# Kernel tuning notes

Hardware: AMD Instinct MI355X
Metric: run time of the kernel (lower is better)

## Reference

```python
import math
import jax, jax.numpy as jnp
import numpy as np

LMAX = 6
SH_DIM = (LMAX + 1) ** 2
NUM_INV = LMAX + 1
SILU_SCALE = 1.0 / 0.6  # ScaledSiLU


def scaled_silu(x):
    return jax.nn.silu(x) * SILU_SCALE


def sph_harm(v):
    """Real spherical harmonics up to LMAX, 'component' normalization, input normalized. [*, 3] -> [*, SH_DIM]."""
    n = jnp.sqrt(jnp.sum(v * v, axis=-1, keepdims=True) + 1e-12)
    v = v / n
    x, y, z = v[..., 0], v[..., 1], v[..., 2]
    st = jnp.sqrt(jnp.clip(x * x + y * y, 0.0, None))  # sin(theta)
    phi = jnp.arctan2(y, x)
    # fully-normalized associated Legendre P[(l,m)] via standard recurrences
    P = {(0, 0): jnp.full_like(z, math.sqrt(1.0 / (4.0 * math.pi)))}
    for m in range(1, LMAX + 1):
        P[(m, m)] = -math.sqrt((2 * m + 1) / (2.0 * m)) * st * P[(m - 1, m - 1)]
    for m in range(0, LMAX):
        P[(m + 1, m)] = math.sqrt(2 * m + 3) * z * P[(m, m)]
    for m in range(0, LMAX + 1):
        for l in range(m + 2, LMAX + 1):
            a = math.sqrt((4 * l * l - 1.0) / (l * l - m * m))
            b = math.sqrt(((l - 1) ** 2 - m * m) / (4.0 * (l - 1) ** 2 - 1.0))
            P[(l, m)] = a * (z * P[(l - 1, m)] - b * P[(l - 2, m)])
    s4pi = math.sqrt(4.0 * math.pi)
    sq2 = math.sqrt(2.0)
    cols = []
    for l in range(LMAX + 1):
        for m in range(-l, l + 1):
            if m < 0:
                cols.append(s4pi * sq2 * P[(l, -m)] * jnp.sin(-m * phi))
            elif m == 0:
                cols.append(s4pi * P[(l, 0)])
            else:
                cols.append(s4pi * sq2 * P[(l, m)] * jnp.cos(m * phi))
    return jnp.stack(cols, axis=-1)


def sh_bilinear_inv(sh1, sh2):
    """Per-l mean of elementwise product. [E, SH_DIM] x2 -> [E, NUM_INV]."""
    outs, idx = [], 0
    for l in range(LMAX + 1):
        d = 2 * l + 1
        outs.append(jnp.mean(sh1[:, idx:idx + d] * sh2[:, idx:idx + d], axis=-1))
        idx += d
    return jnp.stack(outs, axis=-1)


def _forward(node_scalar, node_vector, edge_rbf, edge_udiff, edge_index,
             W_edge, b_edge, W_x1, b_x1, W_x2, b_x2, ln_g, ln_b, W_inv, b_inv):
    H = node_scalar.shape[1]
    N = node_scalar.shape[0]
    j, i = edge_index[0], edge_index[1]
    inv_sqrt3 = 1.0 / math.sqrt(3.0)
    inv_sqrt_h = 1.0 / math.sqrt(H)

    rbf_h = edge_rbf @ W_edge + b_edge  # [E, 3H]

    # scatter-mean of edge directions onto receiving nodes
    counts = jax.ops.segment_sum(jnp.ones_like(i, dtype=edge_udiff.dtype), i, num_segments=N)
    ref_vec = jax.ops.segment_sum(edge_udiff, i, num_segments=N) / jnp.maximum(counts, 1.0)[:, None]
    ref_norm = jnp.sqrt(jnp.sum(ref_vec * ref_vec, axis=-1, keepdims=True) + 1e-9)
    ref_vec = ref_vec / ref_norm
    zero_mask = ref_norm[:, 0] < 5e-5
    default_vec = jnp.array([1.0, 0.0, 0.0], dtype=ref_vec.dtype)
    ref_vec = jnp.where(zero_mask[:, None], default_vec, ref_vec)

    edge_sh = sph_harm(edge_udiff)          # [E, SH_DIM]
    ref_sh = sph_harm(ref_vec)[i]           # [E, SH_DIM]
    inv = sh_bilinear_inv(edge_sh, ref_sh)  # [E, NUM_INV]
    mu = jnp.mean(inv, axis=-1, keepdims=True)
    var = jnp.var(inv, axis=-1, keepdims=True)
    inv = (inv - mu) / jnp.sqrt(var + 1e-5) * ln_g + ln_b

    cos_theta = jnp.sum(edge_udiff * ref_vec[i], axis=-1, keepdims=True)  # [E,1]
    geom = jnp.concatenate([cos_theta, inv], axis=-1)  # [E, NUM_INV+1]
    gate = jnp.tanh(scaled_silu(geom @ W_inv + b_inv))
    rbf_h = rbf_h * (1.0 + gate)

    scalar_proj = scaled_silu(node_scalar @ W_x1 + b_x1) @ W_x2 + b_x2  # [N, 3H]
    x_ji = scalar_proj[j] * rbf_h * inv_sqrt3
    x1, x2, x3 = x_ji[:, :H], x_ji[:, H:2 * H], x_ji[:, 2 * H:]

    vec_ji = (x1[:, None, :] * node_vector[j] + x2[:, None, :] * edge_udiff[:, :, None]) * inv_sqrt_h  # [E,3,H]
    delta_vector = jax.ops.segment_sum(vec_ji, i, num_segments=N)
    delta_scalar = jax.ops.segment_sum(x3, i, num_segments=N)
    return delta_scalar, delta_vector


def setup_inputs() -> dict:
    N, E, H, R = 50000, 400000, 64, 64
    key = jax.random.key(0)
    ks = jax.random.split(key, 16)
    ud = jax.random.normal(ks[3], (E, 3), dtype=jnp.float32)
    ud = ud / jnp.linalg.norm(ud, axis=-1, keepdims=True)
    s = 0.05
    return {
        "node_scalar": jax.random.normal(ks[0], (N, H), dtype=jnp.float32),
        "node_vector": jax.random.normal(ks[1], (N, 3, H), dtype=jnp.float32),
        "edge_rbf": jax.random.uniform(ks[2], (E, R), dtype=jnp.float32),
        "edge_udiff": ud,
        "edge_index": jax.random.randint(ks[4], (2, E), 0, N, dtype=jnp.int32),
        "W_edge": jax.random.normal(ks[5], (R, 3 * H), dtype=jnp.float32) * s,
        "b_edge": jnp.zeros((3 * H,), dtype=jnp.float32),
        "W_x1": jax.random.normal(ks[6], (H, H // 2), dtype=jnp.float32) * s,
        "b_x1": jnp.zeros((H // 2,), dtype=jnp.float32),
        "W_x2": jax.random.normal(ks[7], (H // 2, 3 * H), dtype=jnp.float32) * s,
        "b_x2": jnp.zeros((3 * H,), dtype=jnp.float32),
        "ln_g": jnp.ones((NUM_INV,), dtype=jnp.float32),
        "ln_b": jnp.zeros((NUM_INV,), dtype=jnp.float32),
        "W_inv": jax.random.normal(ks[8], (NUM_INV + 1, 3 * H), dtype=jnp.float32) * s,
        "b_inv": jnp.zeros((3 * H,), dtype=jnp.float32),
    }


def reference(node_scalar, node_vector, edge_rbf, edge_udiff, edge_index,
              W_edge, b_edge, W_x1, b_x1, W_x2, b_x2, ln_g, ln_b, W_inv, b_inv):
    return _forward(node_scalar, node_vector, edge_rbf, edge_udiff, edge_index,
                    W_edge, b_edge, W_x1, b_x1, W_x2, b_x2, ln_g, ln_b, W_inv, b_inv)
```

## Files before the change

kernel.cpp:

```cpp
#include <hip/hip_runtime.h>
#include <math.h>

#define LMAXX 6
#define TPB 256
#define TILE_E 64
#define SCB 256
#define CAPS 12

typedef __attribute__((ext_vector_type(8))) short short8v;
typedef __attribute__((ext_vector_type(16))) float f32x16;
union FragU { short8v v; uint2 u2[2]; };

__device__ __forceinline__ unsigned pack_bf16(float a, float b) {
    unsigned ua = __float_as_uint(a);
    unsigned ub = __float_as_uint(b);
    ua += 0x7fffu + ((ua >> 16) & 1u);
    ub += 0x7fffu + ((ub >> 16) & 1u);
    return (ua >> 16) | (ub & 0xffff0000u);
}
__device__ __forceinline__ float bf16_lo(unsigned w) { return __uint_as_float(w << 16); }
__device__ __forceinline__ float bf16_hi(unsigned w) { return __uint_as_float(w & 0xffff0000u); }

__device__ __forceinline__ void dirang(float x, float y, float z,
                                       float& zo, float& st, float& cphi, float& sphi) {
    float nn = sqrtf(x * x + y * y + z * z + 1e-12f);
    float iv = 1.0f / nn;
    x *= iv; y *= iv; zo = z * iv;
    float st2 = x * x + y * y;
    st = sqrtf(st2 > 0.f ? st2 : 0.f);
    if (st > 1e-30f) { cphi = x / st; sphi = y / st; }
    else { cphi = 1.0f; sphi = 0.0f; }
}

__device__ __forceinline__ void legP(float z, float st, float P[7][7]) {
    P[0][0] = 0.28209479177387814f;
#pragma unroll
    for (int m = 1; m <= LMAXX; ++m)
        P[m][m] = -sqrtf((2.f * m + 1.f) / (2.f * m)) * st * P[m - 1][m - 1];
#pragma unroll
    for (int m = 0; m < LMAXX; ++m)
        P[m + 1][m] = sqrtf(2.f * m + 3.f) * z * P[m][m];
#pragma unroll
    for (int m = 0; m <= LMAXX; ++m) {
#pragma unroll
        for (int l = m + 2; l <= LMAXX; ++l) {
            float a = sqrtf((4.f * l * l - 1.f) / (float)(l * l - m * m));
            float b = sqrtf((float)((l - 1) * (l - 1) - m * m) /
                            (4.f * (l - 1) * (l - 1) - 1.f));
            P[l][m] = a * (z * P[l - 1][m] - b * P[l - 2][m]);
        }
    }
}

__global__ void k_hist(const int* __restrict__ eidx, int* __restrict__ icnt, int E) {
    int e = blockIdx.x * blockDim.x + threadIdx.x;
    if (e >= E) return;
    atomicAdd(&icnt[eidx[E + e]], 1);
}

__global__ void k_scan1(const int* __restrict__ icnt, int* __restrict__ offs,
                        int* __restrict__ bsum, int N) {
    __shared__ int s[SCB];
    int t = threadIdx.x;
    int idx = blockIdx.x * SCB + t;
    int v = (idx < N) ? icnt[idx] : 0;
    s[t] = v; __syncthreads();
#pragma unroll
    for (int off = 1; off < SCB; off <<= 1) {
        int u = (t >= off) ? s[t - off] : 0;
        __syncthreads();
        s[t] += u;
        __syncthreads();
    }
    if (idx < N) offs[idx] = s[t] - v;
    if (t == SCB - 1) bsum[blockIdx.x] = s[t];
}

__global__ void k_scan2(int* __restrict__ bsum, int nb) {
    __shared__ int s[1024];
    int t = threadIdx.x;
    int v = (t < nb) ? bsum[t] : 0;
    s[t] = v; __syncthreads();
#pragma unroll
    for (int off = 1; off < 1024; off <<= 1) {
        int u = (t >= off) ? s[t - off] : 0;
        __syncthreads();
        s[t] += u;
        __syncthreads();
    }
    if (t < nb) bsum[t] = s[t] - v;
}

__global__ void k_scan3(int* __restrict__ offs, const int* __restrict__ bsum,
                        int* __restrict__ cursor, int N) {
    int idx = blockIdx.x * SCB + threadIdx.x;
    if (idx >= N) return;
    int o = offs[idx] + bsum[blockIdx.x];
    offs[idx] = o;
    cursor[idx] = o;
}

__global__ void k_perm(const float* __restrict__ ud, const int* __restrict__ eidx,
                       int* __restrict__ cursor, int* __restrict__ perm,
                       int* __restrict__ ii_s, int* __restrict__ jj_s,
                       float* __restrict__ ud_s, int E) {
    int e = blockIdx.x * blockDim.x + threadIdx.x;
    if (e >= E) return;
    int i = eidx[E + e];
    int j = eidx[e];
    int pos = atomicAdd(&cursor[i], 1);
    perm[pos] = e;
    ii_s[pos] = i;
    jj_s[pos] = j;
    ud_s[3 * pos + 0] = ud[3 * e + 0];
    ud_s[3 * pos + 1] = ud[3 * e + 1];
    ud_s[3 * pos + 2] = ud[3 * e + 2];
}

__global__ void k_node_ref(const int* __restrict__ offs, const int* __restrict__ icnt,
                           const float* __restrict__ ud_s,
                           float* __restrict__ ref_vec, int N) {
    int n = blockIdx.x * blockDim.x + threadIdx.x;
    if (n >= N) return;
    int o0 = offs[n], c = icnt[n];
    float sx = 0.f, sy = 0.f, sz = 0.f;
    for (int e = o0; e < o0 + c; ++e) {
        sx += ud_s[3 * e + 0];
        sy += ud_s[3 * e + 1];
        sz += ud_s[3 * e + 2];
    }
    float d = fmaxf((float)c, 1.0f);
    float vx = sx / d, vy = sy / d, vz = sz / d;
    float norm = sqrtf(vx * vx + vy * vy + vz * vz + 1e-9f);
    float ivn = 1.0f / norm;
    vx *= ivn; vy *= ivn; vz *= ivn;
    if (norm < 5e-5f) { vx = 1.f; vy = 0.f; vz = 0.f; }
    ref_vec[3 * n + 0] = vx;
    ref_vec[3 * n + 1] = vy;
    ref_vec[3 * n + 2] = vz;
}

__global__ __launch_bounds__(TPB) void k_sprojv(const float* __restrict__ ns,
                                                const float* __restrict__ W1,
                                                const float* __restrict__ b1,
                                                const float* __restrict__ W2,
                                                const float* __restrict__ b2,
                                                const float* __restrict__ nvec,
                                                unsigned* __restrict__ gat, int N) {
    __shared__ float sW1[64 * 32];
    __shared__ float sW2[32 * 192];
    __shared__ float sb2[192];
    __shared__ float sb1[32];
    __shared__ float sbuf[4][64];
    __shared__ float h1buf[4][32];
    int t = threadIdx.x;
    for (int p = t; p < 64 * 32; p += TPB) sW1[p] = W1[p];
    for (int p = t; p < 32 * 192; p += TPB) sW2[p] = W2[p];
    if (t < 192) sb2[t] = b2[t];
    if (t < 32) sb1[t] = b1[t];

    int w = t >> 6, l = t & 63;
    int nwaves = gridDim.x * 4;
    int iters = (N + nwaves - 1) / nwaves;
    for (int it = 0; it < iters; ++it) {
        int n = blockIdx.x * 4 + w + it * nwaves;
        bool act = n < N;
        __syncthreads();
        if (act) sbuf[w][l] = ns[(size_t)n * 64 + l];
        __syncthreads();
        if (act) {
            int k = l & 31;
            float h = sb1[k];
#pragma unroll
            for (int c = 0; c < 64; ++c) h = fmaf(sbuf[w][c], sW1[c * 32 + k], h);
            float sig = 1.0f / (1.0f + __expf(-h));
            h = h * sig * (1.0f / 0.6f);
            if (l < 32) h1buf[w][l] = h;
        }
        __syncthreads();
        if (act) {
            float a[3];
#pragma unroll
            for (int m = 0; m < 3; ++m) {
                int o = l + 64 * m;
                float acc = sb2[o];
#pragma unroll
                for (int kk = 0; kk < 32; ++kk)
                    acc = fmaf(h1buf[w][kk], sW2[kk * 192 + o], acc);
                a[m] = acc;
            }
            size_t nb = (size_t)n * 192;
            float nv0 = nvec[nb + l];
            float nv1 = nvec[nb + 64 + l];
            float nv2 = nvec[nb + 128 + l];
            gat[nb + l]        = pack_bf16(a[0], a[1]);
            gat[nb + 64 + l]   = pack_bf16(a[2], nv0);
            gat[nb + 128 + l]  = pack_bf16(nv1, nv2);
        }
    }
}

__global__ void k_geom_s(const float* __restrict__ ud_s, const int* __restrict__ ii_s,
                         const float* __restrict__ ref_vec,
                         const float* __restrict__ ln_g, const float* __restrict__ ln_b,
                         float* __restrict__ geom_s, int E) {
    int r = blockIdx.x * blockDim.x + threadIdx.x;
    if (r >= E) return;
    int i = ii_s[r];
    float ux = ud_s[3 * r], uy = ud_s[3 * r + 1], uz = ud_s[3 * r + 2];
    float rvx = ref_vec[3 * i], rvy = ref_vec[3 * i + 1], rvz = ref_vec[3 * i + 2];

    float zE, stE, cpE, spE, zR, stR, cpR, spR;
    dirang(ux, uy, uz, zE, stE, cpE, spE);
    dirang(rvx, rvy, rvz, zR, stR, cpR, spR);

    float Pe[7][7], Pr[7][7];
    legP(zE, stE, Pe);
    legP(zR, stR, Pr);

    float cmE[7], smE[7], cmR[7], smR[7];
    cmE[0] = 1.f; smE[0] = 0.f; cmE[1] = cpE; smE[1] = spE;
    cmR[0] = 1.f; smR[0] = 0.f; cmR[1] = cpR; smR[1] = spR;
#pragma unroll
    for (int m = 2; m <= LMAXX; ++m) {
        cmE[m] = 2.f * cpE * cmE[m - 1] - cmE[m - 2];
        smE[m] = 2.f * cpE * smE[m - 1] - smE[m - 2];
        cmR[m] = 2.f * cpR * cmR[m - 1] - cmR[m - 2];
        smR[m] = 2.f * cpR * smR[m - 1] - smR[m - 2];
    }

    float inv[7];
#pragma unroll
    for (int l = 0; l <= LMAXX; ++l) inv[l] = Pe[l][0] * Pr[l][0];
#pragma unroll
    for (int m = 1; m <= LMAXX; ++m) {
        float cross = cmE[m] * cmR[m] + smE[m] * smR[m];
#pragma unroll
        for (int l = m; l <= LMAXX; ++l)
            inv[l] += 2.f * Pe[l][m] * Pr[l][m] * cross;
    }
    const float fourpi = 12.566370614359172f;
#pragma unroll
    for (int l = 0; l <= LMAXX; ++l) inv[l] *= fourpi / (float)(2 * l + 1);

    float mu = 0.f;
#pragma unroll
    for (int l = 0; l < 7; ++l) mu += inv[l];
    mu *= (1.0f / 7.0f);
    float var = 0.f;
#pragma unroll
    for (int l = 0; l < 7; ++l) { float d = inv[l] - mu; var += d * d; }
    var *= (1.0f / 7.0f);
    float rstd = rsqrtf(var + 1e-5f);
    float ct = ux * rvx + uy * rvy + uz * rvz;
    float* g = geom_s + (size_t)r * 8;
    g[0] = ct;
#pragma unroll
    for (int l = 0; l < 7; ++l) g[1 + l] = (inv[l] - mu) * rstd * ln_g[l] + ln_b[l];
}

__global__ __launch_bounds__(TPB, 4) void k_main(
    const float* __restrict__ rbf, const float* __restrict__ W_edge,
    const float* __restrict__ b_edge, const float* __restrict__ W_inv,
    const float* __restrict__ b_inv, const float* __restrict__ geom_s,
    const unsigned* __restrict__ gat, const float* __restrict__ ud_s,
    const int* __restrict__ ii_s, const int* __restrict__ jj_s,
    const int* __restrict__ perm,
    float* __restrict__ dscal, float* __restrict__ dvec, int E) {
    __shared__ __align__(16) unsigned sWT[192 * 34];
    __shared__ int sii[64];
    __shared__ int sslot[64];
    __shared__ int sfirst[64];
    __shared__ int sD;
    __shared__ float sacc[CAPS * 256];

    int t = threadIdx.x;
    int l = t & 63;
    int wid = t >> 6;
    int eh = wid >> 1;
    int wc = wid & 1;
    int lo5 = l & 31;
    int hi = l >> 5;
    int h = wc * 32 + lo5;

    for (int p = t; p < 192 * 32; p += TPB) {
        int col = p >> 5, kd = p & 31;
        sWT[col * 34 + kd] = pack_bf16(W_edge[(2 * kd) * 192 + col],
                                       W_edge[(2 * kd + 1) * 192 + col]);
    }

    float wv_inv[8][3];
#pragma unroll
    for (int c = 0; c < 8; ++c)
#pragma unroll
        for (int q = 0; q < 3; ++q)
            wv_inv[c][q] = W_inv[c * 192 + q * 64 + h];
    float bi[3], be[3];
#pragma unroll
    for (int q = 0; q < 3; ++q) {
        bi[q] = b_inv[q * 64 + h];
        be[q] = b_edge[q * 64 + h];
    }

    const float inv_sqrt3 = 0.57735026918962584f;
    const float inv_sqrt_h = 0.125f;

    int ntiles = (E + TILE_E - 1) / TILE_E;
    for (int tile = blockIdx.x; tile < ntiles; tile += gridDim.x) {
        int e0 = tile * TILE_E;
        __syncthreads();
        if (t < 64) {
            int rg = e0 + t;
            sii[t] = (rg < E) ? ii_s[rg] : -1;
        }
        __syncthreads();

        if (t < 64) {
            bool flag = (t == 0) || (sii[t] != sii[t - 1]);
            unsigned long long bal = __ballot(flag);
            unsigned long long mask =
                (t == 63) ? ~0ull : ((1ull << (t + 1)) - 1ull);
            int slot = __popcll(bal & mask) - 1;
            sslot[t] = slot;
            if (flag) sfirst[slot] = t;
            if (t == 0) sD = __popcll(bal);
        }

        FragU afr[4];
        int arow = lo5 + 32 * eh;
        int rga = e0 + arow;
        if (rga < E) {
            int row = perm[rga];
            const float4* rp = (const float4*)&rbf[(size_t)row * 64 + hi * 8];
#pragma unroll
            for (int ks = 0; ks < 4; ++ks) {
                float4 f0 = rp[ks * 4];
                float4 f1 = rp[ks * 4 + 1];
                afr[ks].u2[0] = make_uint2(pack_bf16(f0.x, f0.y), pack_bf16(f0.z, f0.w));
                afr[ks].u2[1] = make_uint2(pack_bf16(f1.x, f1.y), pack_bf16(f1.z, f1.w));
            }
        } else {
#pragma unroll
            for (int ks = 0; ks < 4; ++ks) {
                afr[ks].u2[0] = make_uint2(0u, 0u);
                afr[ks].u2[1] = make_uint2(0u, 0u);
            }
        }

        f32x16 acc0 = {0.f,0.f,0.f,0.f,0.f,0.f,0.f,0.f,0.f,0.f,0.f,0.f,0.f,0.f,0.f,0.f};
        f32x16 acc1 = acc0, acc2 = acc0;
        int bc0 = (wc * 32 + lo5) * 34;
#pragma unroll
        for (int ks = 0; ks < 4; ++ks) {
            int off = ks * 8 + hi * 4;
            FragU b0, b1, b2;
            b0.u2[0] = *(const uint2*)&sWT[bc0 + off];
            b0.u2[1] = *(const uint2*)&sWT[bc0 + off + 2];
            b1.u2[0] = *(const uint2*)&sWT[bc0 + 64 * 34 + off];
            b1.u2[1] = *(const uint2*)&sWT[bc0 + 64 * 34 + off + 2];
            b2.u2[0] = *(const uint2*)&sWT[bc0 + 128 * 34 + off];
            b2.u2[1] = *(const uint2*)&sWT[bc0 + 128 * 34 + off + 2];
            acc0 = __builtin_amdgcn_mfma_f32_32x32x16_bf16(afr[ks].v, b0.v, acc0, 0, 0, 0);
            acc1 = __builtin_amdgcn_mfma_f32_32x32x16_bf16(afr[ks].v, b1.v, acc1, 0, 0, 0);
            acc2 = __builtin_amdgcn_mfma_f32_32x32x16_bf16(afr[ks].v, b2.v, acc2, 0, 0, 0);
        }

        __syncthreads();
        int D = sD;
        bool slotmode = (D <= CAPS);
        if (slotmode) {
            for (int p = t; p < D * 256; p += TPB) sacc[p] = 0.f;
        }
        __syncthreads();

        float a_s = 0.f, a_v0 = 0.f, a_v1 = 0.f, a_v2 = 0.f;
        int runi = -1, runslot = -1;
        auto flush = [&]() {
            if (runi < 0) return;
            if (slotmode) {
                float* sa = &sacc[runslot * 256];
                atomicAdd(&sa[h], a_s);
                atomicAdd(&sa[64 + h], a_v0);
                atomicAdd(&sa[128 + h], a_v1);
                atomicAdd(&sa[192 + h], a_v2);
            } else {
                atomicAdd(&dscal[(size_t)runi * 64 + h], a_s);
                atomicAdd(&dvec[(size_t)runi * 192 + h], a_v0);
                atomicAdd(&dvec[(size_t)runi * 192 + 64 + h], a_v1);
                atomicAdd(&dvec[(size_t)runi * 192 + 128 + h], a_v2);
            }
        };
#pragma unroll
        for (int r = 0; r < 16; ++r) {
            int el = eh * 32 + (r & 3) + 8 * (r >> 2) + 4 * hi;
            int rg = e0 + el;
            if (rg < E) {
                int i = sii[el];
                int j = jj_s[rg];
                if (i != runi) {
                    flush();
                    a_s = 0.f; a_v0 = 0.f; a_v1 = 0.f; a_v2 = 0.f;
                    runi = i; runslot = sslot[el];
                }
                const float4* gp = (const float4*)(geom_s + (size_t)rg * 8);
                float4 g0 = gp[0];
                float4 g1 = gp[1];
                float u0 = bi[0], u1 = bi[1], u2 = bi[2];
                float gg[8] = {g0.x, g0.y, g0.z, g0.w, g1.x, g1.y, g1.z, g1.w};
#pragma unroll
                for (int c = 0; c < 8; ++c) {
                    u0 = fmaf(gg[c], wv_inv[c][0], u0);
                    u1 = fmaf(gg[c], wv_inv[c][1], u1);
                    u2 = fmaf(gg[c], wv_inv[c][2], u2);
                }
                float gate[3];
                float uu[3] = {u0, u1, u2};
#pragma unroll
                for (int q = 0; q < 3; ++q) {
                    float u = uu[q];
                    float sig = 1.0f / (1.0f + __expf(-u));
                    float v = u * sig * (1.0f / 0.6f);
                    v = fminf(fmaxf(v, -20.f), 20.f);
                    float e2v = __expf(2.0f * v);
                    gate[q] = (e2v - 1.0f) / (e2v + 1.0f);
                }
                size_t jb = (size_t)j * 192;
                unsigned w0 = gat[jb + h];
                unsigned w1 = gat[jb + 64 + h];
                unsigned w2 = gat[jb + 128 + h];
                float sp0 = bf16_lo(w0), sp1 = bf16_hi(w0), sp2 = bf16_lo(w1);
                float nv0 = bf16_hi(w1), nv1 = bf16_lo(w2), nv2 = bf16_hi(w2);
                float x1 = sp0 * (acc0[r] + be[0]) * (1.0f + gate[0]) * inv_sqrt3;
                float x2 = sp1 * (acc1[r] + be[1]) * (1.0f + gate[1]) * inv_sqrt3;
                float x3 = sp2 * (acc2[r] + be[2]) * (1.0f + gate[2]) * inv_sqrt3;
                a_s += x3;
                float ud0 = ud_s[3 * rg + 0];
                float ud1 = ud_s[3 * rg + 1];
                float ud2 = ud_s[3 * rg + 2];
                a_v0 += (x1 * nv0 + x2 * ud0) * inv_sqrt_h;
                a_v1 += (x1 * nv1 + x2 * ud1) * inv_sqrt_h;
                a_v2 += (x1 * nv2 + x2 * ud2) * inv_sqrt_h;
            }
        }
        flush();
        __syncthreads();

        if (slotmode) {
            int Dreal = D - ((sii[63] < 0) ? 1 : 0);
            for (int s = 0; s < D; ++s) {
                int n = sii[sfirst[s]];
                if (n < 0) continue;
                float val = sacc[s * 256 + t];
                bool boundary = (s == 0) || (s == Dreal - 1);
                float* ptr = (t < 64) ? &dscal[(size_t)n * 64 + t]
                                      : &dvec[(size_t)n * 192 + (t - 64)];
                if (boundary) atomicAdd(ptr, val);
                else *ptr = val;
            }
        }
    }
}

extern "C" void kernel_launch(void* const* d_in, const int* in_sizes, int n_in,
                              void* d_out, int out_size, void* d_ws, size_t ws_size,
                              hipStream_t stream) {
    const float* node_scalar = (const float*)d_in[0];
    const float* node_vector = (const float*)d_in[1];
    const float* edge_rbf    = (const float*)d_in[2];
    const float* edge_udiff  = (const float*)d_in[3];
    const int*   edge_index  = (const int*)d_in[4];
    const float* W_edge      = (const float*)d_in[5];
    const float* b_edge      = (const float*)d_in[6];
    const float* W_x1        = (const float*)d_in[7];
    const float* b_x1        = (const float*)d_in[8];
    const float* W_x2        = (const float*)d_in[9];
    const float* b_x2        = (const float*)d_in[10];
    const float* ln_g        = (const float*)d_in[11];
    const float* ln_b        = (const float*)d_in[12];
    const float* W_inv       = (const float*)d_in[13];
    const float* b_inv       = (const float*)d_in[14];

    int N = in_sizes[0] / 64;
    int E = in_sizes[3] / 3;

    float* ws = (float*)d_ws;
    size_t o = 0;
    auto A4 = [&]() { o = (o + 3) & ~(size_t)3; };
    int*      icnt   = (int*)(ws + o); o += N; A4();
    int*      offs   = (int*)(ws + o); o += N; A4();
    int*      cursor = (int*)(ws + o); o += N; A4();
    int*      bsum   = (int*)(ws + o); o += 1024; A4();
    float*    ref_vec= ws + o; o += (size_t)N * 3; A4();
    unsigned* gat    = (unsigned*)(ws + o); o += (size_t)N * 192; A4();
    int*      perm   = (int*)(ws + o); o += E; A4();
    float*    geom_s = ws + o; o += (size_t)E * 8; A4();
    float*    ud_s   = ws + o; o += (size_t)E * 3; A4();
    int*      ii_s   = (int*)(ws + o); o += E; A4();
    int*      jj_s   = (int*)(ws + o); o += E; A4();

    float* dscal = (float*)d_out;
    float* dvec  = (float*)d_out + (size_t)N * 64;

    hipMemsetAsync(icnt, 0, (size_t)N * sizeof(int), stream);
    hipMemsetAsync(d_out, 0, (size_t)out_size * sizeof(float), stream);

    int nb = (N + SCB - 1) / SCB;

    k_hist<<<(E + TPB - 1) / TPB, TPB, 0, stream>>>(edge_index, icnt, E);
    k_scan1<<<nb, SCB, 0, stream>>>(icnt, offs, bsum, N);
    k_scan2<<<1, 1024, 0, stream>>>(bsum, nb);
    k_scan3<<<nb, SCB, 0, stream>>>(offs, bsum, cursor, N);
    k_perm<<<(E + TPB - 1) / TPB, TPB, 0, stream>>>(edge_udiff, edge_index, cursor,
                                                    perm, ii_s, jj_s, ud_s, E);
    k_node_ref<<<(N + TPB - 1) / TPB, TPB, 0, stream>>>(offs, icnt, ud_s, ref_vec, N);
    k_sprojv<<<512, TPB, 0, stream>>>(node_scalar, W_x1, b_x1, W_x2, b_x2,
                                      node_vector, gat, N);
    k_geom_s<<<(E + TPB - 1) / TPB, TPB, 0, stream>>>(ud_s, ii_s, ref_vec,
                                                      ln_g, ln_b, geom_s, E);
    k_main<<<1024, TPB, 0, stream>>>(edge_rbf, W_edge, b_edge, W_inv, b_inv, geom_s,
                                     gat, ud_s, ii_s, jj_s, perm, dscal, dvec, E);
}
```

Measured before the change: 576.2 us.

## Compute invariant gate via MFMA and pack per-edge sorted data into structs

Moves the per-edge W_inv projection of the geometric invariants onto bf16 MFMA instructions, computes the gate factors once per tile, and stores them packed as bf16. Geometric features are stored as bf16 instead of fp32. The separate sorted arrays (perm, ii, jj, udiff) are merged into one 32-byte struct per edge so each edge needs fewer scattered loads. A small kernel pre-packs W_inv to bf16. The aim is less redundant per-lane FMA and transcendental work and less memory traffic, at the cost of bf16 precision on the gate and geometry values.

```diff
diff --git a/kernel.cpp b/kernel.cpp
--- a/kernel.cpp
+++ b/kernel.cpp
@@ -9,7 +9,7 @@
 
 typedef __attribute__((ext_vector_type(8))) short short8v;
 typedef __attribute__((ext_vector_type(16))) float f32x16;
-union FragU { short8v v; uint2 u2[2]; };
+union FragU { short8v v; uint2 u2[2]; uint4 u4; };
 
 __device__ __forceinline__ unsigned pack_bf16(float a, float b) {
     unsigned ua = __float_as_uint(a);
@@ -101,33 +101,30 @@
 }
 
 __global__ void k_perm(const float* __restrict__ ud, const int* __restrict__ eidx,
-                       int* __restrict__ cursor, int* __restrict__ perm,
-                       int* __restrict__ ii_s, int* __restrict__ jj_s,
-                       float* __restrict__ ud_s, int E) {
+                       int* __restrict__ cursor, uint4* __restrict__ estr, int E) {
     int e = blockIdx.x * blockDim.x + threadIdx.x;
     if (e >= E) return;
     int i = eidx[E + e];
     int j = eidx[e];
     int pos = atomicAdd(&cursor[i], 1);
-    perm[pos] = e;
-    ii_s[pos] = i;
-    jj_s[pos] = j;
-    ud_s[3 * pos + 0] = ud[3 * e + 0];
-    ud_s[3 * pos + 1] = ud[3 * e + 1];
-    ud_s[3 * pos + 2] = ud[3 * e + 2];
+    estr[2 * pos]     = make_uint4((unsigned)i, (unsigned)e, 0u, 0u);
+    estr[2 * pos + 1] = make_uint4((unsigned)j, __float_as_uint(ud[3 * e + 0]),
+                                   __float_as_uint(ud[3 * e + 1]),
+                                   __float_as_uint(ud[3 * e + 2]));
 }
 
 __global__ void k_node_ref(const int* __restrict__ offs, const int* __restrict__ icnt,
-                           const float* __restrict__ ud_s,
+                           const uint4* __restrict__ estr,
                            float* __restrict__ ref_vec, int N) {
     int n = blockIdx.x * blockDim.x + threadIdx.x;
     if (n >= N) return;
     int o0 = offs[n], c = icnt[n];
     float sx = 0.f, sy = 0.f, sz = 0.f;
     for (int e = o0; e < o0 + c; ++e) {
-        sx += ud_s[3 * e + 0];
-        sy += ud_s[3 * e + 1];
-        sz += ud_s[3 * e + 2];
+        uint4 hi = estr[2 * e + 1];
+        sx += __uint_as_float(hi.y);
+        sy += __uint_as_float(hi.z);
+        sz += __uint_as_float(hi.w);
     }
     float d = fmaxf((float)c, 1.0f);
     float vx = sx / d, vy = sy / d, vz = sz / d;
@@ -200,14 +197,28 @@
     }
 }
 
-__global__ void k_geom_s(const float* __restrict__ ud_s, const int* __restrict__ ii_s,
+__global__ void k_wpk(const float* __restrict__ W_inv, unsigned* __restrict__ wpk) {
+    int idx = blockIdx.x * blockDim.x + threadIdx.x;
+    if (idx >= 192 * 8) return;
+    int col = idx >> 3, p = idx & 7;
+    unsigned v = 0u;
+    if (p < 4)
+        v = pack_bf16(W_inv[(2 * p) * 192 + col], W_inv[(2 * p + 1) * 192 + col]);
+    wpk[col * 8 + p] = v;
+}
+
+__global__ void k_geom_s(const uint4* __restrict__ estr,
                          const float* __restrict__ ref_vec,
                          const float* __restrict__ ln_g, const float* __restrict__ ln_b,
-                         float* __restrict__ geom_s, int E) {
+                         uint4* __restrict__ geom16, int E) {
     int r = blockIdx.x * blockDim.x + threadIdx.x;
     if (r >= E) return;
-    int i = ii_s[r];
-    float ux = ud_s[3 * r], uy = ud_s[3 * r + 1], uz = ud_s[3 * r + 2];
+    uint4 lo = estr[2 * (size_t)r];
+    uint4 hi = estr[2 * (size_t)r + 1];
+    int i = (int)lo.x;
+    float ux = __uint_as_float(hi.y);
+    float uy = __uint_as_float(hi.z);
+    float uz = __uint_as_float(hi.w);
     float rvx = ref_vec[3 * i], rvy = ref_vec[3 * i + 1], rvz = ref_vec[3 * i + 2];
 
     float zE, stE, cpE, spE, zR, stR, cpR, spR;
@@ -253,19 +264,20 @@
     var *= (1.0f / 7.0f);
     float rstd = rsqrtf(var + 1e-5f);
     float ct = ux * rvx + uy * rvy + uz * rvz;
-    float* g = geom_s + (size_t)r * 8;
+    float g[8];
     g[0] = ct;
 #pragma unroll
     for (int l = 0; l < 7; ++l) g[1 + l] = (inv[l] - mu) * rstd * ln_g[l] + ln_b[l];
+    geom16[2 * (size_t)r] = make_uint4(pack_bf16(g[0], g[1]), pack_bf16(g[2], g[3]),
+                                       pack_bf16(g[4], g[5]), pack_bf16(g[6], g[7]));
+    geom16[2 * (size_t)r + 1] = make_uint4(0u, 0u, 0u, 0u);
 }
 
 __global__ __launch_bounds__(TPB, 4) void k_main(
     const float* __restrict__ rbf, const float* __restrict__ W_edge,
-    const float* __restrict__ b_edge, const float* __restrict__ W_inv,
-    const float* __restrict__ b_inv, const float* __restrict__ geom_s,
-    const unsigned* __restrict__ gat, const float* __restrict__ ud_s,
-    const int* __restrict__ ii_s, const int* __restrict__ jj_s,
-    const int* __restrict__ perm,
+    const float* __restrict__ b_edge, const float* __restrict__ b_inv,
+    const unsigned* __restrict__ wpk, const uint4* __restrict__ geom16,
+    const unsigned* __restrict__ gat, const uint4* __restrict__ estr,
     float* __restrict__ dscal, float* __restrict__ dvec, int E) {
     __shared__ __align__(16) unsigned sWT[192 * 34];
     __shared__ int sii[64];
@@ -289,12 +301,10 @@
                                        W_edge[(2 * kd + 1) * 192 + col]);
     }
 
-    float wv_inv[8][3];
-#pragma unroll
-    for (int c = 0; c < 8; ++c)
-#pragma unroll
-        for (int q = 0; q < 3; ++q)
-            wv_inv[c][q] = W_inv[c * 192 + q * 64 + h];
+    FragU bwi[3];
+#pragma unroll
+    for (int q = 0; q < 3; ++q)
+        bwi[q].u4 = *(const uint4*)&wpk[(q * 64 + h) * 8 + hi * 4];
     float bi[3], be[3];
 #pragma unroll
     for (int q = 0; q < 3; ++q) {
@@ -311,7 +321,7 @@
         __syncthreads();
         if (t < 64) {
             int rg = e0 + t;
-            sii[t] = (rg < E) ? ii_s[rg] : -1;
+            sii[t] = (rg < E) ? (int)estr[2 * (size_t)rg].x : -1;
         }
         __syncthreads();
 
@@ -326,11 +336,39 @@
             if (t == 0) sD = __popcll(bal);
         }
 
-        FragU afr[4];
         int arow = lo5 + 32 * eh;
         int rga = e0 + arow;
+
+        unsigned gf[3][8];
+        {
+            FragU ga;
+            if (rga < E) ga.u4 = ((const uint4*)&geom16[2 * (size_t)rga])[hi];
+            else         ga.u4 = make_uint4(0u, 0u, 0u, 0u);
+            f32x16 ug0, ug1, ug2;
+#pragma unroll
+            for (int r = 0; r < 16; ++r) { ug0[r] = bi[0]; ug1[r] = bi[1]; ug2[r] = bi[2]; }
+            ug0 = __builtin_amdgcn_mfma_f32_32x32x16_bf16(ga.v, bwi[0].v, ug0, 0, 0, 0);
+            ug1 = __builtin_amdgcn_mfma_f32_32x32x16_bf16(ga.v, bwi[1].v, ug1, 0, 0, 0);
+            ug2 = __builtin_amdgcn_mfma_f32_32x32x16_bf16(ga.v, bwi[2].v, ug2, 0, 0, 0);
+            auto gfac = [&](float u) -> float {
+                float sig = 1.0f / (1.0f + __expf(-u));
+                float v = u * sig * (1.0f / 0.6f);
+                v = fminf(fmaxf(v, -20.f), 20.f);
+                float e2v = __expf(2.0f * v);
+                float gate = (e2v - 1.0f) / (e2v + 1.0f);
+                return (1.0f + gate) * inv_sqrt3;
+            };
+#pragma unroll
+            for (int rp = 0; rp < 8; ++rp) {
+                gf[0][rp] = pack_bf16(gfac(ug0[2 * rp]), gfac(ug0[2 * rp + 1]));
+                gf[1][rp] = pack_bf16(gfac(ug1[2 * rp]), gfac(ug1[2 * rp + 1]));
+                gf[2][rp] = pack_bf16(gfac(ug2[2 * rp]), gfac(ug2[2 * rp + 1]));
+            }
+        }
+
+        FragU afr[4];
         if (rga < E) {
-            int row = perm[rga];
+            int row = (int)estr[2 * (size_t)rga].y;
             const float4* rp = (const float4*)&rbf[(size_t)row * 64 + hi * 8];
 #pragma unroll
             for (int ks = 0; ks < 4; ++ks) {
@@ -396,47 +434,29 @@
             int rg = e0 + el;
             if (rg < E) {
                 int i = sii[el];
-                int j = jj_s[rg];
                 if (i != runi) {
                     flush();
                     a_s = 0.f; a_v0 = 0.f; a_v1 = 0.f; a_v2 = 0.f;
                     runi = i; runslot = sslot[el];
                 }
-                const float4* gp = (const float4*)(geom_s + (size_t)rg * 8);
-                float4 g0 = gp[0];
-                float4 g1 = gp[1];
-                float u0 = bi[0], u1 = bi[1], u2 = bi[2];
-                float gg[8] = {g0.x, g0.y, g0.z, g0.w, g1.x, g1.y, g1.z, g1.w};
-#pragma unroll
-                for (int c = 0; c < 8; ++c) {
-                    u0 = fmaf(gg[c], wv_inv[c][0], u0);
-                    u1 = fmaf(gg[c], wv_inv[c][1], u1);
-                    u2 = fmaf(gg[c], wv_inv[c][2], u2);
-                }
-                float gate[3];
-                float uu[3] = {u0, u1, u2};
-#pragma unroll
-                for (int q = 0; q < 3; ++q) {
-                    float u = uu[q];
-                    float sig = 1.0f / (1.0f + __expf(-u));
-                    float v = u * sig * (1.0f / 0.6f);
-                    v = fminf(fmaxf(v, -20.f), 20.f);
-                    float e2v = __expf(2.0f * v);
-                    gate[q] = (e2v - 1.0f) / (e2v + 1.0f);
-                }
+                uint4 eh4 = estr[2 * (size_t)rg + 1];
+                int j = (int)eh4.x;
                 size_t jb = (size_t)j * 192;
                 unsigned w0 = gat[jb + h];
                 unsigned w1 = gat[jb + 64 + h];
                 unsigned w2 = gat[jb + 128 + h];
                 float sp0 = bf16_lo(w0), sp1 = bf16_hi(w0), sp2 = bf16_lo(w1);
                 float nv0 = bf16_hi(w1), nv1 = bf16_lo(w2), nv2 = bf16_hi(w2);
-                float x1 = sp0 * (acc0[r] + be[0]) * (1.0f + gate[0]) * inv_sqrt3;
-                float x2 = sp1 * (acc1[r] + be[1]) * (1.0f + gate[1]) * inv_sqrt3;
-                float x3 = sp2 * (acc2[r] + be[2]) * (1.0f + gate[2]) * inv_sqrt3;
+                float gf0 = (r & 1) ? bf16_hi(gf[0][r >> 1]) : bf16_lo(gf[0][r >> 1]);
+                float gf1 = (r & 1) ? bf16_hi(gf[1][r >> 1]) : bf16_lo(gf[1][r >> 1]);
+                float gf2 = (r & 1) ? bf16_hi(gf[2][r >> 1]) : bf16_lo(gf[2][r >> 1]);
+                float x1 = sp0 * (acc0[r] + be[0]) * gf0;
+                float x2 = sp1 * (acc1[r] + be[1]) * gf1;
+                float x3 = sp2 * (acc2[r] + be[2]) * gf2;
                 a_s += x3;
-                float ud0 = ud_s[3 * rg + 0];
-                float ud1 = ud_s[3 * rg + 1];
-                float ud2 = ud_s[3 * rg + 2];
+                float ud0 = __uint_as_float(eh4.y);
+                float ud1 = __uint_as_float(eh4.z);
+                float ud2 = __uint_as_float(eh4.w);
                 a_v0 += (x1 * nv0 + x2 * ud0) * inv_sqrt_h;
                 a_v1 += (x1 * nv1 + x2 * ud1) * inv_sqrt_h;
                 a_v2 += (x1 * nv2 + x2 * ud2) * inv_sqrt_h;
@@ -485,18 +505,16 @@
 
     float* ws = (float*)d_ws;
     size_t o = 0;
-    auto A4 = [&]() { o = (o + 3) & ~(size_t)3; };
-    int*      icnt   = (int*)(ws + o); o += N; A4();
-    int*      offs   = (int*)(ws + o); o += N; A4();
-    int*      cursor = (int*)(ws + o); o += N; A4();
-    int*      bsum   = (int*)(ws + o); o += 1024; A4();
-    float*    ref_vec= ws + o; o += (size_t)N * 3; A4();
-    unsigned* gat    = (unsigned*)(ws + o); o += (size_t)N * 192; A4();
-    int*      perm   = (int*)(ws + o); o += E; A4();
-    float*    geom_s = ws + o; o += (size_t)E * 8; A4();
-    float*    ud_s   = ws + o; o += (size_t)E * 3; A4();
-    int*      ii_s   = (int*)(ws + o); o += E; A4();
-    int*      jj_s   = (int*)(ws + o); o += E; A4();
+    auto A8 = [&]() { o = (o + 7) & ~(size_t)7; };
+    int*      icnt   = (int*)(ws + o); o += N; A8();
+    int*      offs   = (int*)(ws + o); o += N; A8();
+    int*      cursor = (int*)(ws + o); o += N; A8();
+    int*      bsum   = (int*)(ws + o); o += 1024; A8();
+    float*    ref_vec= ws + o; o += (size_t)N * 3; A8();
+    unsigned* gat    = (unsigned*)(ws + o); o += (size_t)N * 192; A8();
+    unsigned* wpk    = (unsigned*)(ws + o); o += 192 * 8; A8();
+    uint4*    estr   = (uint4*)(ws + o); o += (size_t)E * 8; A8();
+    uint4*    geom16 = (uint4*)(ws + o); o += (size_t)E * 8; A8();
 
     float* dscal = (float*)d_out;
     float* dvec  = (float*)d_out + (size_t)N * 64;
@@ -511,12 +529,13 @@
     k_scan2<<<1, 1024, 0, stream>>>(bsum, nb);
     k_scan3<<<nb, SCB, 0, stream>>>(offs, bsum, cursor, N);
     k_perm<<<(E + TPB - 1) / TPB, TPB, 0, stream>>>(edge_udiff, edge_index, cursor,
-                                                    perm, ii_s, jj_s, ud_s, E);
-    k_node_ref<<<(N + TPB - 1) / TPB, TPB, 0, stream>>>(offs, icnt, ud_s, ref_vec, N);
+                                                    estr, E);
+    k_node_ref<<<(N + TPB - 1) / TPB, TPB, 0, stream>>>(offs, icnt, estr, ref_vec, N);
     k_sprojv<<<512, TPB, 0, stream>>>(node_scalar, W_x1, b_x1, W_x2, b_x2,
                                       node_vector, gat, N);
-    k_geom_s<<<(E + TPB - 1) / TPB, TPB, 0, stream>>>(ud_s, ii_s, ref_vec,
-                                                      ln_g, ln_b, geom_s, E);
-    k_main<<<1024, TPB, 0, stream>>>(edge_rbf, W_edge, b_edge, W_inv, b_inv, geom_s,
-                                     gat, ud_s, ii_s, jj_s, perm, dscal, dvec, E);
-}
+    k_wpk<<<(192 * 8 + TPB - 1) / TPB, TPB, 0, stream>>>(W_inv, wpk);
+    k_geom_s<<<(E + TPB - 1) / TPB, TPB, 0, stream>>>(estr, ref_vec, ln_g, ln_b,
+                                                      geom16, E);
+    k_main<<<1024, TPB, 0, stream>>>(edge_rbf, W_edge, b_edge, b_inv, wpk, geom16,
+                                     gat, estr, dscal, dvec, E);
+}
```

Measured after the change: 655.5 us. 1.14x slower.
